# Kernel optimization log

Measured on AMD Instinct MI355X. Metric: run time of the kernel, lower is better.

Reference implementation:

```python
import jax, jax.numpy as jnp
import numpy as np

D_MODEL = 1024
H = 16
D_K = D_MODEL // H
D_FF = 4096
EPS = 1e-6
NEG = -1e9


def setup_inputs() -> dict:
    key = jax.random.key(0)
    ks = jax.random.split(key, 8)
    B, S = 2, 2048
    src = jax.random.normal(ks[0], (B, S, D_MODEL), dtype=jnp.float32)
    src_mask = jnp.ones((B, 1, 1, S), dtype=jnp.int32)
    sc = 1.0 / np.sqrt(D_MODEL)
    wq = jax.random.normal(ks[1], (D_MODEL, D_MODEL), jnp.float32) * sc
    wk = jax.random.normal(ks[2], (D_MODEL, D_MODEL), jnp.float32) * sc
    wv = jax.random.normal(ks[3], (D_MODEL, D_MODEL), jnp.float32) * sc
    wo = jax.random.normal(ks[4], (D_MODEL, D_MODEL), jnp.float32) * sc
    w1 = jax.random.normal(ks[5], (D_FF, D_MODEL), jnp.float32) * sc
    b1 = jnp.zeros((D_FF,), jnp.float32)
    w2 = jax.random.normal(ks[6], (D_MODEL, D_FF), jnp.float32) * (1.0 / np.sqrt(D_FF))
    b2 = jnp.zeros((D_MODEL,), jnp.float32)
    a1 = jnp.ones((1,), jnp.float32)
    be1 = jnp.zeros((1,), jnp.float32)
    a2 = jnp.ones((1,), jnp.float32)
    be2 = jnp.zeros((1,), jnp.float32)
    return dict(src=src, src_mask=src_mask, wq=wq, wk=wk, wv=wv, wo=wo,
                w1=w1, b1=b1, w2=w2, b2=b2, a1=a1, be1=be1, a2=a2, be2=be2)


def layer_norm(x, alpha, bias):
    # torch: mean + unbiased std (ddof=1), eps added to std
    mean = jnp.mean(x, axis=-1, keepdims=True)
    std = jnp.sqrt(jnp.var(x, axis=-1, keepdims=True, ddof=1))
    return alpha * (x - mean) / (std + EPS) + bias


def mha(x, mask, wq, wk, wv, wo):
    B, S, _ = x.shape
    def split(t):  # [B,S,D] -> [B,H,S,D_K]
        return t.reshape(B, S, H, D_K).transpose(0, 2, 1, 3)
    q = split(x @ wq.T)
    k = split(x @ wk.T)
    v = split(x @ wv.T)
    scores = jnp.einsum('bhqd,bhkd->bhqk', q, k) / np.sqrt(D_K)
    scores = jnp.where(mask == 0, NEG, scores)
    attn = jax.nn.softmax(scores, axis=-1)
    out = jnp.einsum('bhqk,bhkd->bhqd', attn, v)
    out = out.transpose(0, 2, 1, 3).reshape(B, S, D_MODEL)
    return out @ wo.T


def reference(src, src_mask, wq, wk, wv, wo, w1, b1, w2, b2, a1, be1, a2, be2):
    x = layer_norm(src, a1, be1)
    src = src + mha(x, src_mask, wq, wk, wv, wo)
    x = layer_norm(src, a2, be2)
    ff = jax.nn.relu(x @ w1.T + b1) @ w2.T + b2
    return src + ff
```

## Files before the change

kernel.cpp:

```cpp
#include <hip/hip_runtime.h>
#include <hip/hip_bf16.h>

typedef unsigned short u16;
typedef unsigned int u32;
typedef float floatx4 __attribute__((ext_vector_type(4)));
typedef __bf16 bf16x8 __attribute__((ext_vector_type(8)));
typedef u16 ushort4v __attribute__((ext_vector_type(4)));
typedef u16 ushort8v __attribute__((ext_vector_type(8)));

#define DEVI static __device__ __forceinline__

DEVI u16 f2bf(float f) {
    u32 u = __builtin_bit_cast(u32, f);
    u += 0x7fffu + ((u >> 16) & 1u);
    return (u16)(u >> 16);
}

DEVI float fexp2(float x) { return __builtin_amdgcn_exp2f(x); }

DEVI void async_cp16(const u16* g, u16* l) {
    __builtin_amdgcn_global_load_lds((const __attribute__((address_space(1))) u32*)g,
                                     (__attribute__((address_space(3))) u32*)l, 16, 0, 0);
}

template<int BM, int BN, int RW, int CW, bool QKV3, bool SPLITK,
         bool BIAS, bool RELU, bool RESID, bool OBF16>
__global__ __launch_bounds__(256) void gemm_nt(
    const u16* __restrict__ A,
    const u16* __restrict__ W0, const u16* __restrict__ W1, const u16* __restrict__ W2,
    const float* __restrict__ bias, const float* __restrict__ resid,
    void* __restrict__ o0, void* __restrict__ o1, void* __restrict__ o2,
    int K, int lda, int Nper, int NX)
{
    static_assert(RW * CW == 4, "4 waves");
    constexpr int WM = BM / RW, WN = BN / CW;
    constexpr int MI = WM / 16, NI = WN / 16;
    __shared__ __align__(16) u16 As[2][BM * 32];
    __shared__ __align__(16) u16 Bs[2][BN * 32];
    const int tid = threadIdx.x;
    const int w = tid >> 6, lane = tid & 63;
    const int q = lane >> 4, ml = lane & 15;
    const int wr = w / CW, wc = w % CW;
    const int m0 = blockIdx.y * BM;
    int bx = blockIdx.x;
    size_t kbase = 0;
    int half = 0;
    if (SPLITK) { half = bx / NX; bx -= half * NX; kbase = (size_t)half * K; }
    int n0 = bx * BN;
    const u16* W = W0;
    void* outp = o0;
    if (QKV3) {
        int sel = n0 / Nper;
        n0 -= sel * Nper;
        W = (sel == 0) ? W0 : (sel == 1 ? W1 : W2);
        outp = (sel == 0) ? o0 : (sel == 1 ? o1 : o2);
    }
    if (SPLITK) outp = half ? o1 : o0;

    auto stage = [&](int buf, int kt) {
#pragma unroll
        for (int p = 0; p < BM / 64; ++p) {
            int g = p * 256 + tid;
            int r = g >> 2, s = g & 3;
            int c = s ^ ((r >> 1) & 3);
            async_cp16(A + (size_t)(m0 + r) * lda + kbase + kt + c * 8,
                       &As[buf][(p * 256 + w * 64) * 8]);
        }
#pragma unroll
        for (int p = 0; p < BN / 64; ++p) {
            int g = p * 256 + tid;
            int r = g >> 2, s = g & 3;
            int c = s ^ ((r >> 1) & 3);
            async_cp16(W + (size_t)(n0 + r) * lda + kbase + kt + c * 8,
                       &Bs[buf][(p * 256 + w * 64) * 8]);
        }
    };

    const floatx4 fzero = {0.f, 0.f, 0.f, 0.f};
    floatx4 acc[MI][NI];
#pragma unroll
    for (int i = 0; i < MI; ++i)
#pragma unroll
        for (int j = 0; j < NI; ++j) acc[i][j] = fzero;

    stage(0, 0);
    for (int it = 0, kt = 0; kt < K; ++it, kt += 32) {
        __syncthreads();
        if (kt + 32 < K) stage((it + 1) & 1, kt + 32);
        const u16* Asb = As[it & 1];
        const u16* Bsb = Bs[it & 1];
        bf16x8 af[MI], bfr[NI];
#pragma unroll
        for (int i = 0; i < MI; ++i) {
            int rm = wr * WM + i * 16 + ml;
            int s = q ^ ((rm >> 1) & 3);
            af[i] = *(const bf16x8*)&Asb[(rm * 4 + s) * 8];
        }
#pragma unroll
        for (int j = 0; j < NI; ++j) {
            int rn = wc * WN + j * 16 + ml;
            int s = q ^ ((rn >> 1) & 3);
            bfr[j] = *(const bf16x8*)&Bsb[(rn * 4 + s) * 8];
        }
#pragma unroll
        for (int i = 0; i < MI; ++i)
#pragma unroll
            for (int j = 0; j < NI; ++j)
                acc[i][j] = __builtin_amdgcn_mfma_f32_16x16x32_bf16(af[i], bfr[j], acc[i][j], 0, 0, 0);
    }

#pragma unroll
    for (int j = 0; j < NI; ++j) {
        int gn = n0 + wc * WN + j * 16 + ml;
        float bj = 0.f;
        if (BIAS) bj = bias[gn];
#pragma unroll
        for (int i = 0; i < MI; ++i) {
            int gm0 = m0 + wr * WM + i * 16 + q * 4;
#pragma unroll
            for (int r = 0; r < 4; ++r) {
                size_t idx = (size_t)(gm0 + r) * Nper + gn;
                float v = acc[i][j][r] + bj;
                if (RELU) v = fmaxf(v, 0.f);
                if (RESID) v += resid[idx];
                if (OBF16) ((u16*)outp)[idx] = f2bf(v);
                else       ((float*)outp)[idx] = v;
            }
        }
    }
}

__global__ __launch_bounds__(128, 2) void flash7(
    const u16* __restrict__ Q, const u16* __restrict__ Kg,
    const u16* __restrict__ Vt, const float* __restrict__ biasv,
    u16* __restrict__ O)
{
    __shared__ __align__(16) u16 Ks[2][64 * 64];
    __shared__ __align__(16) u16 Vs[2][64 * 64];
    const int tid = threadIdx.x;
    const int w = tid >> 6, lane = tid & 63;
    const int q = lane >> 4, ml = lane & 15;
    const int b = blockIdx.y >> 4, h = blockIdx.y & 15;
    const size_t rowQ = (size_t)(b * 2048 + blockIdx.x * 64);
    const float KSC = 0.125f * 1.4426950408889634f;
    const floatx4 fzero = {0.f, 0.f, 0.f, 0.f};

    bf16x8 qa[2][2];
#pragma unroll
    for (int qg = 0; qg < 2; ++qg)
#pragma unroll
        for (int c = 0; c < 2; ++c)
            qa[qg][c] = *(const bf16x8*)&Q[(rowQ + w * 32 + qg * 16 + ml) * 1024
                                           + h * 64 + q * 8 + c * 32];

    auto stage = [&](int buf, int s0) {
#pragma unroll
        for (int p = 0; p < 4; ++p) {
            int L = p * 128 + tid;
            int row = L >> 3, sl = L & 7;
            int ch = sl ^ ((row & 3) | (((row >> 3) & 1) << 2));
            async_cp16(Kg + (size_t)(b * 2048 + s0 + row) * 1024 + h * 64 + ch * 8,
                       &Ks[buf][(p * 128 + w * 64) * 8]);
            async_cp16(Vt + (size_t)(b * 1024 + h * 64 + row) * 2048 + s0 + ch * 8,
                       &Vs[buf][(p * 128 + w * 64) * 8]);
        }
    };

    floatx4 oacc[2][4];
    float lsum[2] = {0.f, 0.f};
#pragma unroll
    for (int qg = 0; qg < 2; ++qg)
#pragma unroll
        for (int d = 0; d < 4; ++d) oacc[qg][d] = fzero;

    const int swk = (ml & 3) | (((ml >> 2) & 1) << 2);
    const int swv = (ml & 3) | (((ml >> 3) & 1) << 2);

    stage(0, 0);
    for (int it = 0; it < 32; ++it) {
        __syncthreads();
        if (it + 1 < 32) stage((it + 1) & 1, (it + 1) * 64);
        const u16* Kb = Ks[it & 1];
        const u16* Vb = Vs[it & 1];
        const int s0 = it * 64;

        bf16x8 pfrag[2][2];
#pragma unroll
        for (int g = 0; g < 2; ++g) {
            const int re = g * 32 + ((ml >> 2) << 3) + (ml & 3);
            bf16x8 ke0 = *(const bf16x8*)&Kb[(re + 0) * 64 + ((0 + q) ^ swk) * 8];
            bf16x8 ke1 = *(const bf16x8*)&Kb[(re + 0) * 64 + ((4 + q) ^ swk) * 8];
            bf16x8 ko0 = *(const bf16x8*)&Kb[(re + 4) * 64 + ((0 + q) ^ swk) * 8];
            bf16x8 ko1 = *(const bf16x8*)&Kb[(re + 4) * 64 + ((4 + q) ^ swk) * 8];
            const float4 be = *(const float4*)&biasv[b * 2048 + s0 + g * 32 + q * 8];
            const float4 bo = *(const float4*)&biasv[b * 2048 + s0 + g * 32 + q * 8 + 4];
#pragma unroll
            for (int qg = 0; qg < 2; ++qg) {
                floatx4 te = fzero, to = fzero;
                te = __builtin_amdgcn_mfma_f32_16x16x32_bf16(ke0, qa[qg][0], te, 0, 0, 0);
                te = __builtin_amdgcn_mfma_f32_16x16x32_bf16(ke1, qa[qg][1], te, 0, 0, 0);
                to = __builtin_amdgcn_mfma_f32_16x16x32_bf16(ko0, qa[qg][0], to, 0, 0, 0);
                to = __builtin_amdgcn_mfma_f32_16x16x32_bf16(ko1, qa[qg][1], to, 0, 0, 0);
                float pe0 = fexp2(fmaf(te[0], KSC, be.x));
                float pe1 = fexp2(fmaf(te[1], KSC, be.y));
                float pe2 = fexp2(fmaf(te[2], KSC, be.z));
                float pe3 = fexp2(fmaf(te[3], KSC, be.w));
                float po0 = fexp2(fmaf(to[0], KSC, bo.x));
                float po1 = fexp2(fmaf(to[1], KSC, bo.y));
                float po2 = fexp2(fmaf(to[2], KSC, bo.z));
                float po3 = fexp2(fmaf(to[3], KSC, bo.w));
                lsum[qg] += ((pe0 + pe1) + (pe2 + pe3)) + ((po0 + po1) + (po2 + po3));
                u32 pk[4];
                pk[0] = ((__builtin_bit_cast(u32, pe0) + 0x8000u) >> 16)
                      | ((__builtin_bit_cast(u32, pe1) + 0x8000u) & 0xffff0000u);
                pk[1] = ((__builtin_bit_cast(u32, pe2) + 0x8000u) >> 16)
                      | ((__builtin_bit_cast(u32, pe3) + 0x8000u) & 0xffff0000u);
                pk[2] = ((__builtin_bit_cast(u32, po0) + 0x8000u) >> 16)
                      | ((__builtin_bit_cast(u32, po1) + 0x8000u) & 0xffff0000u);
                pk[3] = ((__builtin_bit_cast(u32, po2) + 0x8000u) >> 16)
                      | ((__builtin_bit_cast(u32, po3) + 0x8000u) & 0xffff0000u);
                pfrag[g][qg] = __builtin_bit_cast(bf16x8, *(uint4*)pk);
            }
        }
#pragma unroll
        for (int dt = 0; dt < 4; ++dt) {
            int vrow = dt * 16 + ml;
#pragma unroll
            for (int g = 0; g < 2; ++g) {
                bf16x8 vf = *(const bf16x8*)&Vb[vrow * 64 + ((g * 4 + q) ^ swv) * 8];
#pragma unroll
                for (int qg = 0; qg < 2; ++qg)
                    oacc[qg][dt] = __builtin_amdgcn_mfma_f32_16x16x32_bf16(
                        vf, pfrag[g][qg], oacc[qg][dt], 0, 0, 0);
            }
        }
    }
#pragma unroll
    for (int qg = 0; qg < 2; ++qg) {
        float ls = lsum[qg];
        ls += __shfl_xor(ls, 16, 64);
        ls += __shfl_xor(ls, 32, 64);
        const float rcp = 1.f / ls;
        const size_t row = rowQ + w * 32 + qg * 16 + ml;
#pragma unroll
        for (int dt = 0; dt < 4; ++dt)
#pragma unroll
            for (int rp = 0; rp < 4; rp += 2) {
                u32 pk = (u32)f2bf(oacc[qg][dt][rp] * rcp)
                       | ((u32)f2bf(oacc[qg][dt][rp + 1] * rcp) << 16);
                *(u32*)&O[row * 1024 + h * 64 + dt * 16 + q * 4 + rp] = pk;
            }
    }
}

__global__ __launch_bounds__(256) void vtrans(const u16* __restrict__ Vb, u16* __restrict__ Vt)
{
    __shared__ __align__(16) u16 T[64 * 72];
    const int tid = threadIdx.x;
    const int ct = blockIdx.x, rt = blockIdx.y;
    const int b = rt >> 5;
    const int s0 = (rt & 31) * 64;
    const int c0 = ct * 64;
#pragma unroll
    for (int p = 0; p < 2; ++p) {
        int slot = p * 256 + tid;
        int lr = slot >> 3, pc = slot & 7;
        bf16x8 v = *(const bf16x8*)&Vb[(size_t)(b * 2048 + s0 + lr) * 1024 + c0 + pc * 8];
        *(bf16x8*)&T[lr * 72 + pc * 8] = v;
    }
    __syncthreads();
#pragma unroll
    for (int p = 0; p < 2; ++p) {
        int slot = p * 256 + tid;
        int dc = slot >> 3, sc0 = (slot & 7) * 8;
        ushort8v o;
#pragma unroll
        for (int j = 0; j < 8; ++j) o[j] = T[(sc0 + j) * 72 + dc];
        *(ushort8v*)&Vt[(size_t)(b * 1024 + c0 + dc) * 2048 + s0 + sc0] = o;
    }
}

__global__ __launch_bounds__(256) void ln_bf16(const float* __restrict__ x,
    const float* __restrict__ ga, const float* __restrict__ gb, u16* __restrict__ y)
{
    const int row = blockIdx.x, tid = threadIdx.x;
    const float4 v = ((const float4*)(x + (size_t)row * 1024))[tid];
    float s = v.x + v.y + v.z + v.w;
    float ss = v.x * v.x + v.y * v.y + v.z * v.z + v.w * v.w;
#pragma unroll
    for (int d = 1; d < 64; d <<= 1) { s += __shfl_xor(s, d, 64); ss += __shfl_xor(ss, d, 64); }
    __shared__ float ps[4], pss[4];
    const int w = tid >> 6, lane = tid & 63;
    if (lane == 0) { ps[w] = s; pss[w] = ss; }
    __syncthreads();
    s = ps[0] + ps[1] + ps[2] + ps[3];
    ss = pss[0] + pss[1] + pss[2] + pss[3];
    float mean = s * (1.f / 1024.f);
    float var = fmaxf((ss - s * mean) * (1.f / 1023.f), 0.f);
    float sc = ga[0] / (sqrtf(var) + 1e-6f);
    float bb = gb[0];
    ushort4v o;
    o[0] = f2bf((v.x - mean) * sc + bb);
    o[1] = f2bf((v.y - mean) * sc + bb);
    o[2] = f2bf((v.z - mean) * sc + bb);
    o[3] = f2bf((v.w - mean) * sc + bb);
    ((ushort4v*)(y + (size_t)row * 1024))[tid] = o;
}

__global__ __launch_bounds__(256) void cast_all(
    const float* __restrict__ wq, const float* __restrict__ wk,
    const float* __restrict__ wv, const float* __restrict__ wo,
    const float* __restrict__ w1, const float* __restrict__ w2,
    u16* __restrict__ wqb, u16* __restrict__ wkb, u16* __restrict__ wvb,
    u16* __restrict__ wob, u16* __restrict__ w1b, u16* __restrict__ w2b)
{
    size_t i = (size_t)blockIdx.x * 256 + threadIdx.x;
    const float* s; u16* d; size_t off;
    if (i < 262144)       { s = wq; d = wqb; off = i; }
    else if (i < 524288)  { s = wk; d = wkb; off = i - 262144; }
    else if (i < 786432)  { s = wv; d = wvb; off = i - 524288; }
    else if (i < 1048576) { s = wo; d = wob; off = i - 786432; }
    else if (i < 2097152) { s = w1; d = w1b; off = i - 1048576; }
    else                  { s = w2; d = w2b; off = i - 2097152; }
    float4 v = ((const float4*)s)[off];
    ushort4v o = {f2bf(v.x), f2bf(v.y), f2bf(v.z), f2bf(v.w)};
    ((ushort4v*)d)[off] = o;
}

__global__ __launch_bounds__(256) void mask_bias(const int* __restrict__ m, float* __restrict__ bias)
{
    int i = blockIdx.x * 256 + threadIdx.x;
    if (i < 4096) bias[i] = m[i] ? 0.f : -1.442695e9f;
}

__global__ __launch_bounds__(256) void ff2_fin(const float* __restrict__ p0, const float* __restrict__ p1,
    const float* __restrict__ b2, const float* __restrict__ resid, float* __restrict__ out)
{
    const size_t i = (size_t)blockIdx.x * 256 + threadIdx.x;
    float4 a = ((const float4*)p0)[i];
    float4 b = ((const float4*)p1)[i];
    float4 r = ((const float4*)resid)[i];
    float4 bb = ((const float4*)b2)[i & 255];
    float4 o = {a.x + b.x + r.x + bb.x, a.y + b.y + r.y + bb.y,
                a.z + b.z + r.z + bb.z, a.w + b.w + r.w + bb.w};
    ((float4*)out)[i] = o;
}

extern "C" void kernel_launch(void* const* d_in, const int* in_sizes, int n_in,
                              void* d_out, int out_size, void* d_ws, size_t ws_size,
                              hipStream_t stream)
{
    const float* src = (const float*)d_in[0];
    const int* msk   = (const int*)d_in[1];
    const float* wq  = (const float*)d_in[2];
    const float* wk  = (const float*)d_in[3];
    const float* wv  = (const float*)d_in[4];
    const float* wo  = (const float*)d_in[5];
    const float* w1  = (const float*)d_in[6];
    const float* b1  = (const float*)d_in[7];
    const float* w2  = (const float*)d_in[8];
    const float* b2  = (const float*)d_in[9];
    const float* a1  = (const float*)d_in[10];
    const float* be1 = (const float*)d_in[11];
    const float* a2  = (const float*)d_in[12];
    const float* be2 = (const float*)d_in[13];
    float* out = (float*)d_out;

    char* ws = (char*)d_ws;
    const size_t MB = (size_t)1 << 20;
    u16* wqb  = (u16*)(ws + 0 * MB);
    u16* wkb  = (u16*)(ws + 2 * MB);
    u16* wvb  = (u16*)(ws + 4 * MB);
    u16* wob  = (u16*)(ws + 6 * MB);
    u16* w1b  = (u16*)(ws + 8 * MB);
    u16* w2b  = (u16*)(ws + 16 * MB);
    u16* xln1 = (u16*)(ws + 24 * MB);
    u16* attn = xln1;
    u16* Qb   = (u16*)(ws + 32 * MB);
    u16* xln2 = Qb;
    u16* Kb   = (u16*)(ws + 40 * MB);
    u16* Vb   = (u16*)(ws + 48 * MB);
    u16* Vt   = (u16*)(ws + 56 * MB);
    float* biasv = (float*)(ws + 64 * MB);
    u16* h1   = (u16*)(ws + 40 * MB);
    float* src2 = (float*)(ws + 72 * MB);
    float* P0 = (float*)(ws + 0 * MB);
    float* P1 = (float*)(ws + 24 * MB);

    cast_all<<<12288, 256, 0, stream>>>(wq, wk, wv, wo, w1, w2,
                                        wqb, wkb, wvb, wob, w1b, w2b);
    mask_bias<<<16, 256, 0, stream>>>(msk, biasv);

    ln_bf16<<<4096, 256, 0, stream>>>(src, a1, be1, xln1);

    gemm_nt<128, 128, 2, 2, true, false, false, false, false, true><<<dim3(24, 32), 256, 0, stream>>>(
        xln1, wqb, wkb, wvb, nullptr, nullptr, Qb, Kb, Vb, 1024, 1024, 1024, 0);

    vtrans<<<dim3(16, 64), 256, 0, stream>>>(Vb, Vt);

    flash7<<<dim3(32, 32), 128, 0, stream>>>(Qb, Kb, Vt, biasv, attn);

    gemm_nt<128, 64, 4, 1, false, false, false, false, true, false><<<dim3(16, 32), 256, 0, stream>>>(
        attn, wob, nullptr, nullptr, nullptr, src, src2, nullptr, nullptr, 1024, 1024, 1024, 0);

    ln_bf16<<<4096, 256, 0, stream>>>(src2, a2, be2, xln2);

    gemm_nt<128, 128, 2, 2, false, false, true, true, false, true><<<dim3(32, 32), 256, 0, stream>>>(
        xln2, w1b, nullptr, nullptr, b1, nullptr, h1, nullptr, nullptr, 1024, 1024, 4096, 0);

    gemm_nt<128, 128, 2, 2, false, true, false, false, false, false><<<dim3(16, 32), 256, 0, stream>>>(
        h1, w2b, nullptr, nullptr, nullptr, nullptr, P0, P1, nullptr, 2048, 4096, 1024, 8);

    ff2_fin<<<4096, 256, 0, stream>>>(P0, P1, b2, src2, out);
}
```

Baseline: 365.2 us.

## Split attention KV range across two blocks and fuse prep kernels

The flash attention kernel now processes half of the key sequence per block (grid z=2). Each half writes unnormalized bf16 partial outputs plus per-row softmax sums, and a new attn_fin kernel adds the halves and normalizes. This doubles the number of attention blocks, aiming to fill the GPU better than 1024 small blocks do. Separately, the weight cast, mask bias and first layernorm are merged into one prep launch to save launch overhead. The cost is an extra kernel, extra global traffic for the partials, and an extra bf16 rounding of the unnormalized partial outputs.

```diff
diff --git a/kernel.cpp b/kernel.cpp
--- a/kernel.cpp
+++ b/kernel.cpp
@@ -15,6 +15,7 @@
     u += 0x7fffu + ((u >> 16) & 1u);
     return (u16)(u >> 16);
 }
+DEVI float bf2f(u16 h) { return __builtin_bit_cast(float, (u32)h << 16); }
 
 DEVI float fexp2(float x) { return __builtin_amdgcn_exp2f(x); }
 
@@ -130,10 +131,10 @@
     }
 }
 
-__global__ __launch_bounds__(128, 2) void flash7(
+__global__ __launch_bounds__(128, 2) void flash8(
     const u16* __restrict__ Q, const u16* __restrict__ Kg,
     const u16* __restrict__ Vt, const float* __restrict__ biasv,
-    u16* __restrict__ O)
+    u16* __restrict__ O0, u16* __restrict__ O1, float* __restrict__ Lp)
 {
     __shared__ __align__(16) u16 Ks[2][64 * 64];
     __shared__ __align__(16) u16 Vs[2][64 * 64];
@@ -141,6 +142,8 @@
     const int w = tid >> 6, lane = tid & 63;
     const int q = lane >> 4, ml = lane & 15;
     const int b = blockIdx.y >> 4, h = blockIdx.y & 15;
+    const int half = blockIdx.z;
+    const int kb = half * 1024;
     const size_t rowQ = (size_t)(b * 2048 + blockIdx.x * 64);
     const float KSC = 0.125f * 1.4426950408889634f;
     const floatx4 fzero = {0.f, 0.f, 0.f, 0.f};
@@ -176,13 +179,13 @@
     const int swk = (ml & 3) | (((ml >> 2) & 1) << 2);
     const int swv = (ml & 3) | (((ml >> 3) & 1) << 2);
 
-    stage(0, 0);
-    for (int it = 0; it < 32; ++it) {
+    stage(0, kb);
+    for (int it = 0; it < 16; ++it) {
         __syncthreads();
-        if (it + 1 < 32) stage((it + 1) & 1, (it + 1) * 64);
+        if (it + 1 < 16) stage((it + 1) & 1, kb + (it + 1) * 64);
         const u16* Kb = Ks[it & 1];
         const u16* Vb = Vs[it & 1];
-        const int s0 = it * 64;
+        const int s0 = kb + it * 64;
 
         bf16x8 pfrag[2][2];
 #pragma unroll
@@ -235,22 +238,45 @@
             }
         }
     }
+    u16* Op = half ? O1 : O0;
 #pragma unroll
     for (int qg = 0; qg < 2; ++qg) {
         float ls = lsum[qg];
         ls += __shfl_xor(ls, 16, 64);
         ls += __shfl_xor(ls, 32, 64);
-        const float rcp = 1.f / ls;
+        const int qs = blockIdx.x * 64 + w * 32 + qg * 16 + ml;
+        if (q == 0)
+            Lp[(((half * 2 + b) * 16) + h) * 2048 + qs] = ls;
         const size_t row = rowQ + w * 32 + qg * 16 + ml;
 #pragma unroll
-        for (int dt = 0; dt < 4; ++dt)
-#pragma unroll
-            for (int rp = 0; rp < 4; rp += 2) {
-                u32 pk = (u32)f2bf(oacc[qg][dt][rp] * rcp)
-                       | ((u32)f2bf(oacc[qg][dt][rp + 1] * rcp) << 16);
-                *(u32*)&O[row * 1024 + h * 64 + dt * 16 + q * 4 + rp] = pk;
-            }
-    }
+        for (int dt = 0; dt < 4; ++dt) {
+            u32 pk0 = (u32)f2bf(oacc[qg][dt][0]) | ((u32)f2bf(oacc[qg][dt][1]) << 16);
+            u32 pk1 = (u32)f2bf(oacc[qg][dt][2]) | ((u32)f2bf(oacc[qg][dt][3]) << 16);
+            u32 pk[2] = {pk0, pk1};
+            *(ushort4v*)&Op[row * 1024 + h * 64 + dt * 16 + q * 4] =
+                __builtin_bit_cast(ushort4v, *(ulong1*)pk);
+        }
+    }
+}
+
+__global__ __launch_bounds__(256) void attn_fin(
+    const u16* __restrict__ O0, const u16* __restrict__ O1,
+    const float* __restrict__ Lp, u16* __restrict__ attn)
+{
+    const int row = blockIdx.x;
+    const int b = row >> 11, qs = row & 2047;
+    const int c0 = threadIdx.x * 4;
+    const int h = c0 >> 6;
+    float l0 = Lp[((b * 16) + h) * 2048 + qs];
+    float l1 = Lp[(((2 + b) * 16) + h) * 2048 + qs];
+    float rcp = 1.f / (l0 + l1);
+    ushort4v a = *(const ushort4v*)&O0[(size_t)row * 1024 + c0];
+    ushort4v bb = *(const ushort4v*)&O1[(size_t)row * 1024 + c0];
+    ushort4v o;
+#pragma unroll
+    for (int i = 0; i < 4; ++i)
+        o[i] = f2bf((bf2f(a[i]) + bf2f(bb[i])) * rcp);
+    *(ushort4v*)&attn[(size_t)row * 1024 + c0] = o;
 }
 
 __global__ __launch_bounds__(256) void vtrans(const u16* __restrict__ Vb, u16* __restrict__ Vt)
@@ -280,10 +306,9 @@
     }
 }
 
-__global__ __launch_bounds__(256) void ln_bf16(const float* __restrict__ x,
-    const float* __restrict__ ga, const float* __restrict__ gb, u16* __restrict__ y)
-{
-    const int row = blockIdx.x, tid = threadIdx.x;
+DEVI void ln_row(const float* __restrict__ x, float ga, float gb,
+                 u16* __restrict__ y, int row, int tid)
+{
     const float4 v = ((const float4*)(x + (size_t)row * 1024))[tid];
     float s = v.x + v.y + v.z + v.w;
     float ss = v.x * v.x + v.y * v.y + v.z * v.z + v.w * v.w;
@@ -297,40 +322,50 @@
     ss = pss[0] + pss[1] + pss[2] + pss[3];
     float mean = s * (1.f / 1024.f);
     float var = fmaxf((ss - s * mean) * (1.f / 1023.f), 0.f);
-    float sc = ga[0] / (sqrtf(var) + 1e-6f);
-    float bb = gb[0];
+    float sc = ga / (sqrtf(var) + 1e-6f);
     ushort4v o;
-    o[0] = f2bf((v.x - mean) * sc + bb);
-    o[1] = f2bf((v.y - mean) * sc + bb);
-    o[2] = f2bf((v.z - mean) * sc + bb);
-    o[3] = f2bf((v.w - mean) * sc + bb);
+    o[0] = f2bf((v.x - mean) * sc + gb);
+    o[1] = f2bf((v.y - mean) * sc + gb);
+    o[2] = f2bf((v.z - mean) * sc + gb);
+    o[3] = f2bf((v.w - mean) * sc + gb);
     ((ushort4v*)(y + (size_t)row * 1024))[tid] = o;
 }
 
-__global__ __launch_bounds__(256) void cast_all(
+__global__ __launch_bounds__(256) void ln_bf16(const float* __restrict__ x,
+    const float* __restrict__ ga, const float* __restrict__ gb, u16* __restrict__ y)
+{
+    ln_row(x, ga[0], gb[0], y, blockIdx.x, threadIdx.x);
+}
+
+__global__ __launch_bounds__(256) void prep(
     const float* __restrict__ wq, const float* __restrict__ wk,
     const float* __restrict__ wv, const float* __restrict__ wo,
     const float* __restrict__ w1, const float* __restrict__ w2,
     u16* __restrict__ wqb, u16* __restrict__ wkb, u16* __restrict__ wvb,
-    u16* __restrict__ wob, u16* __restrict__ w1b, u16* __restrict__ w2b)
-{
-    size_t i = (size_t)blockIdx.x * 256 + threadIdx.x;
-    const float* s; u16* d; size_t off;
-    if (i < 262144)       { s = wq; d = wqb; off = i; }
-    else if (i < 524288)  { s = wk; d = wkb; off = i - 262144; }
-    else if (i < 786432)  { s = wv; d = wvb; off = i - 524288; }
-    else if (i < 1048576) { s = wo; d = wob; off = i - 786432; }
-    else if (i < 2097152) { s = w1; d = w1b; off = i - 1048576; }
-    else                  { s = w2; d = w2b; off = i - 2097152; }
-    float4 v = ((const float4*)s)[off];
-    ushort4v o = {f2bf(v.x), f2bf(v.y), f2bf(v.z), f2bf(v.w)};
-    ((ushort4v*)d)[off] = o;
-}
-
-__global__ __launch_bounds__(256) void mask_bias(const int* __restrict__ m, float* __restrict__ bias)
-{
-    int i = blockIdx.x * 256 + threadIdx.x;
-    if (i < 4096) bias[i] = m[i] ? 0.f : -1.442695e9f;
+    u16* __restrict__ wob, u16* __restrict__ w1b, u16* __restrict__ w2b,
+    const int* __restrict__ m, float* __restrict__ biasv,
+    const float* __restrict__ src, const float* __restrict__ a1,
+    const float* __restrict__ be1, u16* __restrict__ xln1)
+{
+    const int bx = blockIdx.x;
+    if (bx < 12288) {
+        size_t i = (size_t)bx * 256 + threadIdx.x;
+        const float* s; u16* d; size_t off;
+        if (i < 262144)       { s = wq; d = wqb; off = i; }
+        else if (i < 524288)  { s = wk; d = wkb; off = i - 262144; }
+        else if (i < 786432)  { s = wv; d = wvb; off = i - 524288; }
+        else if (i < 1048576) { s = wo; d = wob; off = i - 786432; }
+        else if (i < 2097152) { s = w1; d = w1b; off = i - 1048576; }
+        else                  { s = w2; d = w2b; off = i - 2097152; }
+        float4 v = ((const float4*)s)[off];
+        ushort4v o = {f2bf(v.x), f2bf(v.y), f2bf(v.z), f2bf(v.w)};
+        ((ushort4v*)d)[off] = o;
+    } else if (bx < 12304) {
+        int i = (bx - 12288) * 256 + threadIdx.x;
+        biasv[i] = m[i] ? 0.f : -1.442695e9f;
+    } else {
+        ln_row(src, a1[0], be1[0], xln1, bx - 12304, threadIdx.x);
+    }
 }
 
 __global__ __launch_bounds__(256) void ff2_fin(const float* __restrict__ p0, const float* __restrict__ p1,
@@ -384,21 +419,23 @@
     float* biasv = (float*)(ws + 64 * MB);
     u16* h1   = (u16*)(ws + 40 * MB);
     float* src2 = (float*)(ws + 72 * MB);
+    u16* Oh0  = (u16*)(ws + 48 * MB);
+    u16* Oh1  = (u16*)(ws + 72 * MB);
+    float* Lp = (float*)(ws + 80 * MB);
     float* P0 = (float*)(ws + 0 * MB);
     float* P1 = (float*)(ws + 24 * MB);
 
-    cast_all<<<12288, 256, 0, stream>>>(wq, wk, wv, wo, w1, w2,
-                                        wqb, wkb, wvb, wob, w1b, w2b);
-    mask_bias<<<16, 256, 0, stream>>>(msk, biasv);
-
-    ln_bf16<<<4096, 256, 0, stream>>>(src, a1, be1, xln1);
+    prep<<<16400, 256, 0, stream>>>(wq, wk, wv, wo, w1, w2,
+                                    wqb, wkb, wvb, wob, w1b, w2b,
+                                    msk, biasv, src, a1, be1, xln1);
 
     gemm_nt<128, 128, 2, 2, true, false, false, false, false, true><<<dim3(24, 32), 256, 0, stream>>>(
         xln1, wqb, wkb, wvb, nullptr, nullptr, Qb, Kb, Vb, 1024, 1024, 1024, 0);
 
     vtrans<<<dim3(16, 64), 256, 0, stream>>>(Vb, Vt);
 
-    flash7<<<dim3(32, 32), 128, 0, stream>>>(Qb, Kb, Vt, biasv, attn);
+    flash8<<<dim3(32, 32, 2), 128, 0, stream>>>(Qb, Kb, Vt, biasv, Oh0, Oh1, Lp);
+    attn_fin<<<4096, 256, 0, stream>>>(Oh0, Oh1, Lp, attn);
 
     gemm_nt<128, 64, 4, 1, false, false, false, false, true, false><<<dim3(16, 32), 256, 0, stream>>>(
         attn, wob, nullptr, nullptr, nullptr, src, src2, nullptr, nullptr, 1024, 1024, 1024, 0);
```

New measurement: 378.5 us. 3.6% more time.

## Use 4-way split-K with bf16 partials for FF2 and fuse prep kernels

Applied to the files above, without the earlier changes.

The FF2 GEMM now splits K four ways instead of two. This doubles the grid to 1024 blocks for better CU occupancy, and the partial sums are written as bf16 instead of fp32, so less partial traffic goes through memory. The weight cast, mask-bias and first layernorm are merged into one prep launch to save launch gaps. Rounding the partial sums to bf16 before the final reduction adds precision error to the output.

```diff
diff --git a/kernel.cpp b/kernel.cpp
--- a/kernel.cpp
+++ b/kernel.cpp
@@ -15,6 +15,7 @@
     u += 0x7fffu + ((u >> 16) & 1u);
     return (u16)(u >> 16);
 }
+DEVI float bf2f(u16 h) { return __builtin_bit_cast(float, (u32)h << 16); }
 
 DEVI float fexp2(float x) { return __builtin_amdgcn_exp2f(x); }
 
@@ -23,14 +24,14 @@
                                      (__attribute__((address_space(3))) u32*)l, 16, 0, 0);
 }
 
-template<int BM, int BN, int RW, int CW, bool QKV3, bool SPLITK,
+template<int BM, int BN, int RW, int CW, bool QKV3, int NSPLIT,
          bool BIAS, bool RELU, bool RESID, bool OBF16>
 __global__ __launch_bounds__(256) void gemm_nt(
     const u16* __restrict__ A,
     const u16* __restrict__ W0, const u16* __restrict__ W1, const u16* __restrict__ W2,
     const float* __restrict__ bias, const float* __restrict__ resid,
     void* __restrict__ o0, void* __restrict__ o1, void* __restrict__ o2,
-    int K, int lda, int Nper, int NX)
+    void* __restrict__ o3, int K, int lda, int Nper, int NX)
 {
     static_assert(RW * CW == 4, "4 waves");
     constexpr int WM = BM / RW, WN = BN / CW;
@@ -44,18 +45,19 @@
     const int m0 = blockIdx.y * BM;
     int bx = blockIdx.x;
     size_t kbase = 0;
-    int half = 0;
-    if (SPLITK) { half = bx / NX; bx -= half * NX; kbase = (size_t)half * K; }
-    int n0 = bx * BN;
     const u16* W = W0;
     void* outp = o0;
+    if (NSPLIT > 1) {
+        int part = bx / NX; bx -= part * NX; kbase = (size_t)part * K;
+        outp = (part == 0) ? o0 : (part == 1 ? o1 : (part == 2 ? o2 : o3));
+    }
+    int n0 = bx * BN;
     if (QKV3) {
         int sel = n0 / Nper;
         n0 -= sel * Nper;
         W = (sel == 0) ? W0 : (sel == 1 ? W1 : W2);
         outp = (sel == 0) ? o0 : (sel == 1 ? o1 : o2);
     }
-    if (SPLITK) outp = half ? o1 : o0;
 
     auto stage = [&](int buf, int kt) {
 #pragma unroll
@@ -280,10 +282,9 @@
     }
 }
 
-__global__ __launch_bounds__(256) void ln_bf16(const float* __restrict__ x,
-    const float* __restrict__ ga, const float* __restrict__ gb, u16* __restrict__ y)
-{
-    const int row = blockIdx.x, tid = threadIdx.x;
+DEVI void ln_row(const float* __restrict__ x, float ga, float gb,
+                 u16* __restrict__ y, int row, int tid)
+{
     const float4 v = ((const float4*)(x + (size_t)row * 1024))[tid];
     float s = v.x + v.y + v.z + v.w;
     float ss = v.x * v.x + v.y * v.y + v.z * v.z + v.w * v.w;
@@ -297,52 +298,70 @@
     ss = pss[0] + pss[1] + pss[2] + pss[3];
     float mean = s * (1.f / 1024.f);
     float var = fmaxf((ss - s * mean) * (1.f / 1023.f), 0.f);
-    float sc = ga[0] / (sqrtf(var) + 1e-6f);
-    float bb = gb[0];
+    float sc = ga / (sqrtf(var) + 1e-6f);
     ushort4v o;
-    o[0] = f2bf((v.x - mean) * sc + bb);
-    o[1] = f2bf((v.y - mean) * sc + bb);
-    o[2] = f2bf((v.z - mean) * sc + bb);
-    o[3] = f2bf((v.w - mean) * sc + bb);
+    o[0] = f2bf((v.x - mean) * sc + gb);
+    o[1] = f2bf((v.y - mean) * sc + gb);
+    o[2] = f2bf((v.z - mean) * sc + gb);
+    o[3] = f2bf((v.w - mean) * sc + gb);
     ((ushort4v*)(y + (size_t)row * 1024))[tid] = o;
 }
 
-__global__ __launch_bounds__(256) void cast_all(
+__global__ __launch_bounds__(256) void ln_bf16(const float* __restrict__ x,
+    const float* __restrict__ ga, const float* __restrict__ gb, u16* __restrict__ y)
+{
+    ln_row(x, ga[0], gb[0], y, blockIdx.x, threadIdx.x);
+}
+
+__global__ __launch_bounds__(256) void prep(
     const float* __restrict__ wq, const float* __restrict__ wk,
     const float* __restrict__ wv, const float* __restrict__ wo,
     const float* __restrict__ w1, const float* __restrict__ w2,
     u16* __restrict__ wqb, u16* __restrict__ wkb, u16* __restrict__ wvb,
-    u16* __restrict__ wob, u16* __restrict__ w1b, u16* __restrict__ w2b)
-{
-    size_t i = (size_t)blockIdx.x * 256 + threadIdx.x;
-    const float* s; u16* d; size_t off;
-    if (i < 262144)       { s = wq; d = wqb; off = i; }
-    else if (i < 524288)  { s = wk; d = wkb; off = i - 262144; }
-    else if (i < 786432)  { s = wv; d = wvb; off = i - 524288; }
-    else if (i < 1048576) { s = wo; d = wob; off = i - 786432; }
-    else if (i < 2097152) { s = w1; d = w1b; off = i - 1048576; }
-    else                  { s = w2; d = w2b; off = i - 2097152; }
-    float4 v = ((const float4*)s)[off];
-    ushort4v o = {f2bf(v.x), f2bf(v.y), f2bf(v.z), f2bf(v.w)};
-    ((ushort4v*)d)[off] = o;
-}
-
-__global__ __launch_bounds__(256) void mask_bias(const int* __restrict__ m, float* __restrict__ bias)
-{
-    int i = blockIdx.x * 256 + threadIdx.x;
-    if (i < 4096) bias[i] = m[i] ? 0.f : -1.442695e9f;
-}
-
-__global__ __launch_bounds__(256) void ff2_fin(const float* __restrict__ p0, const float* __restrict__ p1,
-    const float* __restrict__ b2, const float* __restrict__ resid, float* __restrict__ out)
+    u16* __restrict__ wob, u16* __restrict__ w1b, u16* __restrict__ w2b,
+    const int* __restrict__ m, float* __restrict__ biasv,
+    const float* __restrict__ src, const float* __restrict__ a1,
+    const float* __restrict__ be1, u16* __restrict__ xln1)
+{
+    const int bx = blockIdx.x;
+    if (bx < 12288) {
+        size_t i = (size_t)bx * 256 + threadIdx.x;
+        const float* s; u16* d; size_t off;
+        if (i < 262144)       { s = wq; d = wqb; off = i; }
+        else if (i < 524288)  { s = wk; d = wkb; off = i - 262144; }
+        else if (i < 786432)  { s = wv; d = wvb; off = i - 524288; }
+        else if (i < 1048576) { s = wo; d = wob; off = i - 786432; }
+        else if (i < 2097152) { s = w1; d = w1b; off = i - 1048576; }
+        else                  { s = w2; d = w2b; off = i - 2097152; }
+        float4 v = ((const float4*)s)[off];
+        ushort4v o = {f2bf(v.x), f2bf(v.y), f2bf(v.z), f2bf(v.w)};
+        ((ushort4v*)d)[off] = o;
+    } else if (bx < 12304) {
+        int i = (bx - 12288) * 256 + threadIdx.x;
+        biasv[i] = m[i] ? 0.f : -1.442695e9f;
+    } else {
+        ln_row(src, a1[0], be1[0], xln1, bx - 12304, threadIdx.x);
+    }
+}
+
+__global__ __launch_bounds__(256) void ff2_fin(
+    const u16* __restrict__ p0, const u16* __restrict__ p1,
+    const u16* __restrict__ p2, const u16* __restrict__ p3,
+    const float* __restrict__ b2, const float* __restrict__ resid,
+    float* __restrict__ out)
 {
     const size_t i = (size_t)blockIdx.x * 256 + threadIdx.x;
-    float4 a = ((const float4*)p0)[i];
-    float4 b = ((const float4*)p1)[i];
+    ushort4v a = *(const ushort4v*)&p0[i * 4];
+    ushort4v b = *(const ushort4v*)&p1[i * 4];
+    ushort4v c = *(const ushort4v*)&p2[i * 4];
+    ushort4v d = *(const ushort4v*)&p3[i * 4];
     float4 r = ((const float4*)resid)[i];
     float4 bb = ((const float4*)b2)[i & 255];
-    float4 o = {a.x + b.x + r.x + bb.x, a.y + b.y + r.y + bb.y,
-                a.z + b.z + r.z + bb.z, a.w + b.w + r.w + bb.w};
+    float4 o;
+    o.x = (bf2f(a[0]) + bf2f(b[0])) + (bf2f(c[0]) + bf2f(d[0])) + r.x + bb.x;
+    o.y = (bf2f(a[1]) + bf2f(b[1])) + (bf2f(c[1]) + bf2f(d[1])) + r.y + bb.y;
+    o.z = (bf2f(a[2]) + bf2f(b[2])) + (bf2f(c[2]) + bf2f(d[2])) + r.z + bb.z;
+    o.w = (bf2f(a[3]) + bf2f(b[3])) + (bf2f(c[3]) + bf2f(d[3])) + r.w + bb.w;
     ((float4*)out)[i] = o;
 }
 
@@ -384,32 +403,35 @@
     float* biasv = (float*)(ws + 64 * MB);
     u16* h1   = (u16*)(ws + 40 * MB);
     float* src2 = (float*)(ws + 72 * MB);
-    float* P0 = (float*)(ws + 0 * MB);
-    float* P1 = (float*)(ws + 24 * MB);
-
-    cast_all<<<12288, 256, 0, stream>>>(wq, wk, wv, wo, w1, w2,
-                                        wqb, wkb, wvb, wob, w1b, w2b);
-    mask_bias<<<16, 256, 0, stream>>>(msk, biasv);
-
-    ln_bf16<<<4096, 256, 0, stream>>>(src, a1, be1, xln1);
-
-    gemm_nt<128, 128, 2, 2, true, false, false, false, false, true><<<dim3(24, 32), 256, 0, stream>>>(
-        xln1, wqb, wkb, wvb, nullptr, nullptr, Qb, Kb, Vb, 1024, 1024, 1024, 0);
+    u16* P0 = (u16*)(ws + 0 * MB);
+    u16* P1 = (u16*)(ws + 8 * MB);
+    u16* P2 = (u16*)(ws + 24 * MB);
+    u16* P3 = (u16*)(ws + 32 * MB);
+
+    prep<<<16400, 256, 0, stream>>>(wq, wk, wv, wo, w1, w2,
+                                    wqb, wkb, wvb, wob, w1b, w2b,
+                                    msk, biasv, src, a1, be1, xln1);
+
+    gemm_nt<128, 128, 2, 2, true, 1, false, false, false, true><<<dim3(24, 32), 256, 0, stream>>>(
+        xln1, wqb, wkb, wvb, nullptr, nullptr, Qb, Kb, Vb, nullptr, 1024, 1024, 1024, 0);
 
     vtrans<<<dim3(16, 64), 256, 0, stream>>>(Vb, Vt);
 
     flash7<<<dim3(32, 32), 128, 0, stream>>>(Qb, Kb, Vt, biasv, attn);
 
-    gemm_nt<128, 64, 4, 1, false, false, false, false, true, false><<<dim3(16, 32), 256, 0, stream>>>(
-        attn, wob, nullptr, nullptr, nullptr, src, src2, nullptr, nullptr, 1024, 1024, 1024, 0);
+    gemm_nt<128, 64, 4, 1, false, 1, false, false, true, false><<<dim3(16, 32), 256, 0, stream>>>(
+        attn, wob, nullptr, nullptr, nullptr, src, src2, nullptr, nullptr, nullptr,
+        1024, 1024, 1024, 0);
 
     ln_bf16<<<4096, 256, 0, stream>>>(src2, a2, be2, xln2);
 
-    gemm_nt<128, 128, 2, 2, false, false, true, true, false, true><<<dim3(32, 32), 256, 0, stream>>>(
-        xln2, w1b, nullptr, nullptr, b1, nullptr, h1, nullptr, nullptr, 1024, 1024, 4096, 0);
-
-    gemm_nt<128, 128, 2, 2, false, true, false, false, false, false><<<dim3(16, 32), 256, 0, stream>>>(
-        h1, w2b, nullptr, nullptr, nullptr, nullptr, P0, P1, nullptr, 2048, 4096, 1024, 8);
-
-    ff2_fin<<<4096, 256, 0, stream>>>(P0, P1, b2, src2, out);
-}
+    gemm_nt<128, 128, 2, 2, false, 1, true, true, false, true><<<dim3(32, 32), 256, 0, stream>>>(
+        xln2, w1b, nullptr, nullptr, b1, nullptr, h1, nullptr, nullptr, nullptr,
+        1024, 1024, 4096, 0);
+
+    gemm_nt<128, 128, 2, 2, false, 4, false, false, false, true><<<dim3(32, 32), 256, 0, stream>>>(
+        h1, w2b, nullptr, nullptr, nullptr, nullptr, P0, P1, P2, P3,
+        1024, 4096, 1024, 8);
+
+    ff2_fin<<<4096, 256, 0, stream>>>(P0, P1, P2, P3, b2, src2, out);
+}
```

New measurement: 369.0 us. No clear change (+1.0%).
